# Optimization experiments

Measured on AMD Instinct MI355X. Metric: run time of the kernel, lower is better.

## Reference

```python
import math
import jax, jax.numpy as jnp
import numpy as np

B, C, M = 32, 1024, 1024
D, DV, R_ANCHOR = 512, 512, 64


def setup_inputs() -> dict:
    key = jax.random.key(0)
    ks = jax.random.split(key, 6)
    return {
        "T": jax.random.normal(ks[0], (B, C, M), dtype=jnp.float32),
        "Wq": jax.random.normal(ks[1], (C, D), dtype=jnp.float32) * 0.02,
        "Wk": jax.random.normal(ks[2], (C, D), dtype=jnp.float32) * 0.02,
        "Wv": jax.random.normal(ks[3], (C, DV), dtype=jnp.float32) * 0.02,
        "Wout": jax.random.normal(ks[4], (DV, C), dtype=jnp.float32) * 0.02,
        "R_full": jax.random.normal(ks[5], (R_ANCHOR, M), dtype=jnp.float32) * 0.02,
    }


def reference(T, Wq, Wk, Wv, Wout, R_full):
    # T: [B, C, m] -> tokens-major [B, m, C]
    b, c, m = T.shape
    T_mC = jnp.swapaxes(T, 1, 2)
    Q = T_mC @ Wq           # [B, m, D]
    K = T_mC @ Wk           # [B, m, D]
    V = T_mC @ Wv           # [B, m, DV]
    Rm = R_full[:, :m]      # [r, m]
    # Faithful to original torch einsum: m and j are summed INDEPENDENTLY
    # (outer product of row-sums of R with token-sums of K/V), not contracted.
    K_proj = jnp.einsum('rm,bjd->brd', Rm, K)   # [B, r, D]
    V_proj = jnp.einsum('rm,bjd->brd', Rm, V)   # [B, r, DV]
    scale = 1.0 / math.sqrt(max(1.0, float(Wq.shape[1])))
    scores = jnp.einsum('bid,btd->bit', Q, K_proj) * scale  # [B, m, r]
    A = jax.nn.softmax(scores, axis=-1)
    T_out_mdv = jnp.einsum('bir,brd->bid', A, V_proj)       # [B, m, DV]
    T_out_C = T_out_mdv @ Wout                               # [B, m, C]
    return jnp.swapaxes(T_out_C, 1, 2)                       # [B, C, m]
```

## Files before the change

### kernel.cpp

```cpp
#include <hip/hip_runtime.h>
#include <math.h>

constexpr int Bc  = 32;
constexpr int Cc  = 1024;
constexpr int Mc  = 1024;
constexpr int Dc  = 512;
constexpr int DVc = 512;
constexpr int Rc  = 64;

typedef float f4 __attribute__((ext_vector_type(4)));

__global__ __launch_bounds__(256) void k_kv1(const float* __restrict__ T,
                                             const float* __restrict__ Wk,
                                             const float* __restrict__ Wv,
                                             float* __restrict__ pK,
                                             float* __restrict__ pV) {
    __shared__ float  ts[32];
    __shared__ float4 kp[2][128];
    __shared__ float4 vp[2][128];

    const int cs  = blockIdx.x;
    const int b   = blockIdx.y;
    const int c0  = cs * 32;
    const int tid = threadIdx.x;
    const int w   = tid >> 6, lane = tid & 63;

    const float* Tb = T + ((long)b * Cc + c0 + w * 8) * Mc + lane * 4;
    float racc[8];
#pragma unroll
    for (int rp = 0; rp < 4; ++rp) {
        const float* r0 = Tb + (long)(2 * rp) * Mc;
        const float* r1 = r0 + Mc;
        float4 a[4], c[4];
#pragma unroll
        for (int k = 0; k < 4; ++k) a[k] = *(const float4*)&r0[k * 256];
#pragma unroll
        for (int k = 0; k < 4; ++k) c[k] = *(const float4*)&r1[k * 256];
        float s0 = 0.f, s1 = 0.f;
#pragma unroll
        for (int k = 0; k < 4; ++k) {
            s0 += (a[k].x + a[k].y) + (a[k].z + a[k].w);
            s1 += (c[k].x + c[k].y) + (c[k].z + c[k].w);
        }
        racc[2 * rp] = s0;
        racc[2 * rp + 1] = s1;
    }
#pragma unroll
    for (int off = 32; off; off >>= 1) {
#pragma unroll
        for (int r = 0; r < 8; ++r) racc[r] += __shfl_down(racc[r], off, 64);
    }
    if (lane == 0) {
#pragma unroll
        for (int r = 0; r < 8; ++r) ts[w * 8 + r] = racc[r];
    }
    __syncthreads();

    const int tq = tid >> 7, tr = tid & 127;
    const float4* Wk4 = (const float4*)(Wk + (long)c0 * Dc) + tr;
    const float4* Wv4 = (const float4*)(Wv + (long)c0 * DVc) + tr;
    float4 ka = {0.f, 0.f, 0.f, 0.f}, va = {0.f, 0.f, 0.f, 0.f};
#pragma unroll 4
    for (int j = 0; j < 16; ++j) {
        const int c = j * 2 + tq;
        const float t = ts[c];
        float4 wk = Wk4[(long)c * 128];
        float4 wv = Wv4[(long)c * 128];
        ka.x = fmaf(t, wk.x, ka.x); ka.y = fmaf(t, wk.y, ka.y);
        ka.z = fmaf(t, wk.z, ka.z); ka.w = fmaf(t, wk.w, ka.w);
        va.x = fmaf(t, wv.x, va.x); va.y = fmaf(t, wv.y, va.y);
        va.z = fmaf(t, wv.z, va.z); va.w = fmaf(t, wv.w, va.w);
    }
    kp[tq][tr] = ka;
    vp[tq][tr] = va;
    __syncthreads();

    const long base = ((long)b * 32 + cs) * 512;
    if (tid < 128) {
        float4 s0 = kp[0][tid], s1 = kp[1][tid];
        float4 s = {s0.x + s1.x, s0.y + s1.y, s0.z + s1.z, s0.w + s1.w};
        ((float4*)(pK + base))[tid] = s;
    } else {
        const int t2 = tid - 128;
        float4 s0 = vp[0][t2], s1 = vp[1][t2];
        float4 s = {s0.x + s1.x, s0.y + s1.y, s0.z + s1.z, s0.w + s1.w};
        ((float4*)(pV + base))[t2] = s;
    }
}

__global__ __launch_bounds__(256) void k_kv2r(const float* __restrict__ pK,
                                              const float* __restrict__ pV,
                                              float* __restrict__ Ksum,
                                              float* __restrict__ Vsum,
                                              const float* __restrict__ Rfull,
                                              float* __restrict__ rsum) {
    if (blockIdx.x < 128) {
        const int gid = blockIdx.x * 256 + threadIdx.x;
        const int sel = gid >> 14;
        const int rem = gid & 16383;
        const float* p = (sel ? pV : pK) + (long)(rem >> 9) * 32 * 512 + (rem & 511);
        float v[32];
#pragma unroll
        for (int i = 0; i < 32; ++i) v[i] = p[i * 512];
        float s = 0.f;
#pragma unroll
        for (int i = 0; i < 32; ++i) s += v[i];
        (sel ? Vsum : Ksum)[rem] = s;
    } else {
        const int row  = (blockIdx.x - 128) * 4 + (threadIdx.x >> 6);
        const int lane = threadIdx.x & 63;
        const float* xr = Rfull + (long)row * 1024;
        float s = 0.f;
#pragma unroll
        for (int k = 0; k < 4; ++k) {
            float4 t = *(const float4*)&xr[k * 256 + lane * 4];
            s += (t.x + t.y) + (t.z + t.w);
        }
#pragma unroll
        for (int off = 32; off; off >>= 1) s += __shfl_down(s, off, 64);
        if (lane == 0) rsum[row] = s;
    }
}

__global__ __launch_bounds__(256) void k_mid(const float* __restrict__ Wq,
                                             const float* __restrict__ Ksum,
                                             float* __restrict__ wqk,
                                             const float* __restrict__ Wout,
                                             const float* __restrict__ Vsum,
                                             float* __restrict__ pVW) {
    __shared__ float vs[64];
    if (blockIdx.x < 8192) {
        const int wid  = blockIdx.x * 4 + (threadIdx.x >> 6);
        const int lane = threadIdx.x & 63;
        const float* wq = Wq + (long)(wid & 1023) * Dc;
        const float* ks = Ksum + (wid >> 10) * Dc;
        float s = 0.f;
#pragma unroll
        for (int k = 0; k < 4; ++k) {
            int d = k * 128 + lane * 2;
            float2 a = *(const float2*)&wq[d];
            float2 x = *(const float2*)&ks[d];
            s = fmaf(a.x, x.x, s);
            s = fmaf(a.y, x.y, s);
        }
#pragma unroll
        for (int off = 32; off; off >>= 1) s += __shfl_down(s, off, 64);
        if (lane == 0) wqk[wid] = s;
    } else {
        const int idx = blockIdx.x - 8192;
        const int ds  = idx & 7;
        const int b   = idx >> 3;
        const int d0  = ds * 64;
        const int tid = threadIdx.x;
        if (tid < 64) vs[tid] = Vsum[b * Dc + d0 + tid];
        __syncthreads();
        float a0 = 0.f, a1 = 0.f, a2 = 0.f, a3 = 0.f;
        const float* W0 = Wout + (long)d0 * Cc + tid;
#pragma unroll 4
        for (int d = 0; d < 64; ++d) {
            float v = vs[d];
            const float* wr = W0 + (long)d * Cc;
            a0 = fmaf(v, wr[0],   a0);
            a1 = fmaf(v, wr[256], a1);
            a2 = fmaf(v, wr[512], a2);
            a3 = fmaf(v, wr[768], a3);
        }
        const long base = ((long)b * 8 + ds) * 1024 + tid;
        pVW[base] = a0;  pVW[base + 256] = a1;
        pVW[base + 512] = a2;  pVW[base + 768] = a3;
    }
}

__global__ __launch_bounds__(256) void k_final(const float* __restrict__ T,
                                               const float* __restrict__ wqk,
                                               const float* __restrict__ pVW,
                                               const float* __restrict__ rsum,
                                               float* __restrict__ Out,
                                               float scale) {
    __shared__ float rs[64];
    __shared__ float part[32][40];
    __shared__ float wsh[32];
    __shared__ float wql[Cc];
    __shared__ float vwl[Cc];

    const int b   = blockIdx.y;
    const int m0  = blockIdx.x * 32;
    const int tid = threadIdx.x;
    const int il  = tid & 7;
    const int cs  = tid >> 3;

    ((float4*)wql)[tid] = ((const float4*)(wqk + b * Cc))[tid];
#pragma unroll
    for (int c = tid; c < Cc; c += 256) {
        const float* p = pVW + (long)b * 8 * 1024 + c;
        float v[8];
#pragma unroll
        for (int j = 0; j < 8; ++j) v[j] = p[j * 1024];
        float s = 0.f;
#pragma unroll
        for (int j = 0; j < 8; ++j) s += v[j];
        vwl[c] = s;
    }
    if (tid < 64) rs[tid] = rsum[tid];
    __syncthreads();

    const float* Tbm = T + (long)b * Cc * Mc + m0 + il * 4;
    float4 acc = make_float4(0.f, 0.f, 0.f, 0.f);
#pragma unroll
    for (int cb = 0; cb < 4; ++cb) {
        float4 t[8];
#pragma unroll
        for (int u = 0; u < 8; ++u)
            t[u] = *(const float4*)&Tbm[(long)(cs + (cb * 8 + u) * 32) * Mc];
#pragma unroll
        for (int u = 0; u < 8; ++u) {
            const float wc = wql[cs + (cb * 8 + u) * 32];
            acc.x = fmaf(t[u].x, wc, acc.x);
            acc.y = fmaf(t[u].y, wc, acc.y);
            acc.z = fmaf(t[u].z, wc, acc.z);
            acc.w = fmaf(t[u].w, wc, acc.w);
        }
    }
    *(float4*)&part[cs][il * 4] = acc;
    __syncthreads();

    if (tid < 32) {
        const int i = tid;
        float q = 0.f;
#pragma unroll
        for (int k = 0; k < 32; ++k) q += part[k][i];
        q *= scale;
        float mx = -1e30f;
#pragma unroll
        for (int r = 0; r < 64; ++r) mx = fmaxf(mx, q * rs[r]);
        float se = 0.f, sw = 0.f;
#pragma unroll
        for (int r = 0; r < 64; ++r) {
            float e = __expf(q * rs[r] - mx);
            se += e;
            sw = fmaf(e, rs[r], sw);
        }
        wsh[i] = sw / se;
    }
    __syncthreads();

    float* Ob = Out + (long)b * Cc * Mc + m0 + il * 4;
    float4 w4 = *(const float4*)&wsh[il * 4];
#pragma unroll 4
    for (int c = cs; c < Cc; c += 32) {
        float v = vwl[c];
        f4 o = {w4.x * v, w4.y * v, w4.z * v, w4.w * v};
        __builtin_nontemporal_store(o, (f4*)&Ob[(long)c * Mc]);
    }
}

extern "C" void kernel_launch(void* const* d_in, const int* in_sizes, int n_in,
                              void* d_out, int out_size, void* d_ws, size_t ws_size,
                              hipStream_t stream) {
    const float* T     = (const float*)d_in[0];
    const float* Wq    = (const float*)d_in[1];
    const float* Wk    = (const float*)d_in[2];
    const float* Wv    = (const float*)d_in[3];
    const float* Wout  = (const float*)d_in[4];
    const float* Rfull = (const float*)d_in[5];
    float* Out = (float*)d_out;

    float* ws   = (float*)d_ws;
    float* rsum = ws;
    float* Ksum = rsum + Rc;
    float* Vsum = Ksum + Bc * Dc;
    float* wqk  = Vsum + Bc * DVc;
    float* vw   = wqk + Bc * Cc;
    float* pK   = vw + Bc * Cc;
    float* pV   = pK + 524288;
    float* pVW  = pV + 524288;

    k_kv1<<<dim3(32, Bc), 256, 0, stream>>>(T, Wk, Wv, pK, pV);
    k_kv2r<<<144, 256, 0, stream>>>(pK, pV, Ksum, Vsum, Rfull, rsum);
    k_mid<<<8448, 256, 0, stream>>>(Wq, Ksum, wqk, Wout, Vsum, pVW);
    const float scale = 1.0f / sqrtf((float)Dc);
    k_final<<<dim3(Mc / 32, Bc), 256, 0, stream>>>(T, wqk, pVW, rsum, Out, scale);
}
```

Measured before the change: 285.8 us.

## Fuse KV reduction and mid-stage matvecs into one kernel, drop nontemporal stores

Merges the partial K/V sum reduction, the R row-sum, the Wq·Ksum matvec and the Vsum·Wout matvec into a single kernel with a (9, B) grid. Each block recomputes the per-batch K/V sums in shared memory, so no Ksum/Vsum or pVW partial buffers make a global round trip, and one launch is removed. k_final now loads a finished vw vector instead of summing 8 partials. The final output store also switches from nontemporal to ordinary stores. In exchange, the fused kernel redundantly reduces pK/pV eight times per batch and runs only 288 blocks, which may underuse the GPU.

```diff
diff --git a/kernel.cpp b/kernel.cpp
--- a/kernel.cpp
+++ b/kernel.cpp
@@ -7,8 +7,6 @@
 constexpr int Dc  = 512;
 constexpr int DVc = 512;
 constexpr int Rc  = 64;
-
-typedef float f4 __attribute__((ext_vector_type(4)));
 
 __global__ __launch_bounds__(256) void k_kv1(const float* __restrict__ T,
                                              const float* __restrict__ Wk,
@@ -88,92 +86,122 @@
     }
 }
 
-__global__ __launch_bounds__(256) void k_kv2r(const float* __restrict__ pK,
+__global__ __launch_bounds__(256) void k_mid2(const float* __restrict__ pK,
                                               const float* __restrict__ pV,
-                                              float* __restrict__ Ksum,
-                                              float* __restrict__ Vsum,
+                                              const float* __restrict__ Wq,
+                                              const float* __restrict__ Wout,
                                               const float* __restrict__ Rfull,
+                                              float* __restrict__ wqk,
+                                              float* __restrict__ vw,
                                               float* __restrict__ rsum) {
-    if (blockIdx.x < 128) {
-        const int gid = blockIdx.x * 256 + threadIdx.x;
-        const int sel = gid >> 14;
-        const int rem = gid & 16383;
-        const float* p = (sel ? pV : pK) + (long)(rem >> 9) * 32 * 512 + (rem & 511);
+    __shared__ float Ks[512];
+    __shared__ float Vs[512];
+    __shared__ float pvw[256];
+
+    const int j   = blockIdx.x;
+    const int b   = blockIdx.y;
+    const int tid = threadIdx.x;
+    const int w   = tid >> 6, lane = tid & 63;
+
+    if (j == 8) {
+        if (w < 2) {
+            const int row = 2 * b + w;
+            const float* xr = Rfull + (long)row * 1024;
+            float s = 0.f;
+#pragma unroll
+            for (int k = 0; k < 4; ++k) {
+                float4 t = *(const float4*)&xr[k * 256 + lane * 4];
+                s += (t.x + t.y) + (t.z + t.w);
+            }
+#pragma unroll
+            for (int off = 32; off; off >>= 1) s += __shfl_down(s, off, 64);
+            if (lane == 0) rsum[row] = s;
+        }
+        return;
+    }
+
+    {
+        const float* pKb = pK + (long)b * 32 * 512;
+        const float* pVb = pV + (long)b * 32 * 512;
         float v[32];
 #pragma unroll
-        for (int i = 0; i < 32; ++i) v[i] = p[i * 512];
+        for (int i = 0; i < 32; ++i) v[i] = pKb[i * 512 + tid];
         float s = 0.f;
 #pragma unroll
         for (int i = 0; i < 32; ++i) s += v[i];
-        (sel ? Vsum : Ksum)[rem] = s;
-    } else {
-        const int row  = (blockIdx.x - 128) * 4 + (threadIdx.x >> 6);
-        const int lane = threadIdx.x & 63;
-        const float* xr = Rfull + (long)row * 1024;
-        float s = 0.f;
-#pragma unroll
-        for (int k = 0; k < 4; ++k) {
-            float4 t = *(const float4*)&xr[k * 256 + lane * 4];
-            s += (t.x + t.y) + (t.z + t.w);
-        }
-#pragma unroll
-        for (int off = 32; off; off >>= 1) s += __shfl_down(s, off, 64);
-        if (lane == 0) rsum[row] = s;
-    }
-}
-
-__global__ __launch_bounds__(256) void k_mid(const float* __restrict__ Wq,
-                                             const float* __restrict__ Ksum,
-                                             float* __restrict__ wqk,
-                                             const float* __restrict__ Wout,
-                                             const float* __restrict__ Vsum,
-                                             float* __restrict__ pVW) {
-    __shared__ float vs[64];
-    if (blockIdx.x < 8192) {
-        const int wid  = blockIdx.x * 4 + (threadIdx.x >> 6);
-        const int lane = threadIdx.x & 63;
-        const float* wq = Wq + (long)(wid & 1023) * Dc;
-        const float* ks = Ksum + (wid >> 10) * Dc;
-        float s = 0.f;
-#pragma unroll
-        for (int k = 0; k < 4; ++k) {
-            int d = k * 128 + lane * 2;
-            float2 a = *(const float2*)&wq[d];
-            float2 x = *(const float2*)&ks[d];
-            s = fmaf(a.x, x.x, s);
-            s = fmaf(a.y, x.y, s);
-        }
-#pragma unroll
-        for (int off = 32; off; off >>= 1) s += __shfl_down(s, off, 64);
-        if (lane == 0) wqk[wid] = s;
-    } else {
-        const int idx = blockIdx.x - 8192;
-        const int ds  = idx & 7;
-        const int b   = idx >> 3;
-        const int d0  = ds * 64;
-        const int tid = threadIdx.x;
-        if (tid < 64) vs[tid] = Vsum[b * Dc + d0 + tid];
+        Ks[tid] = s;
+#pragma unroll
+        for (int i = 0; i < 32; ++i) v[i] = pKb[i * 512 + tid + 256];
+        s = 0.f;
+#pragma unroll
+        for (int i = 0; i < 32; ++i) s += v[i];
+        Ks[tid + 256] = s;
+#pragma unroll
+        for (int i = 0; i < 32; ++i) v[i] = pVb[i * 512 + tid];
+        s = 0.f;
+#pragma unroll
+        for (int i = 0; i < 32; ++i) s += v[i];
+        Vs[tid] = s;
+#pragma unroll
+        for (int i = 0; i < 32; ++i) v[i] = pVb[i * 512 + tid + 256];
+        s = 0.f;
+#pragma unroll
+        for (int i = 0; i < 32; ++i) s += v[i];
+        Vs[tid + 256] = s;
+    }
+    __syncthreads();
+
+    const int c0 = j * 128;
+
+    {
+        float myKs[8];
+#pragma unroll
+        for (int k = 0; k < 8; ++k) myKs[k] = Ks[lane + k * 64];
+        const int cbase = c0 + w * 32;
+#pragma unroll
+        for (int bt = 0; bt < 4; ++bt) {
+            float p[8];
+#pragma unroll
+            for (int u = 0; u < 8; ++u) {
+                const float* wqr = Wq + (long)(cbase + bt * 8 + u) * Dc + lane;
+                float acc = 0.f;
+#pragma unroll
+                for (int k = 0; k < 8; ++k) acc = fmaf(wqr[k * 64], myKs[k], acc);
+                p[u] = acc;
+            }
+#pragma unroll
+            for (int off = 32; off; off >>= 1) {
+#pragma unroll
+                for (int u = 0; u < 8; ++u) p[u] += __shfl_down(p[u], off, 64);
+            }
+            if (lane == 0) {
+#pragma unroll
+                for (int u = 0; u < 8; ++u) wqk[b * Cc + cbase + bt * 8 + u] = p[u];
+            }
+        }
+    }
+
+    {
+        const int ci = tid & 127, h = tid >> 7;
+        const float* W0 = Wout + (long)(h * 256) * Cc + c0 + ci;
+        float acc = 0.f;
+#pragma unroll 4
+        for (int d0 = 0; d0 < 256; d0 += 8) {
+            float w8[8];
+#pragma unroll
+            for (int q = 0; q < 8; ++q) w8[q] = W0[(long)(d0 + q) * Cc];
+#pragma unroll
+            for (int q = 0; q < 8; ++q) acc = fmaf(Vs[h * 256 + d0 + q], w8[q], acc);
+        }
+        pvw[tid] = acc;
         __syncthreads();
-        float a0 = 0.f, a1 = 0.f, a2 = 0.f, a3 = 0.f;
-        const float* W0 = Wout + (long)d0 * Cc + tid;
-#pragma unroll 4
-        for (int d = 0; d < 64; ++d) {
-            float v = vs[d];
-            const float* wr = W0 + (long)d * Cc;
-            a0 = fmaf(v, wr[0],   a0);
-            a1 = fmaf(v, wr[256], a1);
-            a2 = fmaf(v, wr[512], a2);
-            a3 = fmaf(v, wr[768], a3);
-        }
-        const long base = ((long)b * 8 + ds) * 1024 + tid;
-        pVW[base] = a0;  pVW[base + 256] = a1;
-        pVW[base + 512] = a2;  pVW[base + 768] = a3;
+        if (tid < 128) vw[b * Cc + c0 + tid] = pvw[tid] + pvw[tid + 128];
     }
 }
 
 __global__ __launch_bounds__(256) void k_final(const float* __restrict__ T,
                                                const float* __restrict__ wqk,
-                                               const float* __restrict__ pVW,
+                                               const float* __restrict__ vw,
                                                const float* __restrict__ rsum,
                                                float* __restrict__ Out,
                                                float scale) {
@@ -190,17 +218,7 @@
     const int cs  = tid >> 3;
 
     ((float4*)wql)[tid] = ((const float4*)(wqk + b * Cc))[tid];
-#pragma unroll
-    for (int c = tid; c < Cc; c += 256) {
-        const float* p = pVW + (long)b * 8 * 1024 + c;
-        float v[8];
-#pragma unroll
-        for (int j = 0; j < 8; ++j) v[j] = p[j * 1024];
-        float s = 0.f;
-#pragma unroll
-        for (int j = 0; j < 8; ++j) s += v[j];
-        vwl[c] = s;
-    }
+    ((float4*)vwl)[tid] = ((const float4*)(vw  + b * Cc))[tid];
     if (tid < 64) rs[tid] = rsum[tid];
     __syncthreads();
 
@@ -249,8 +267,8 @@
 #pragma unroll 4
     for (int c = cs; c < Cc; c += 32) {
         float v = vwl[c];
-        f4 o = {w4.x * v, w4.y * v, w4.z * v, w4.w * v};
-        __builtin_nontemporal_store(o, (f4*)&Ob[(long)c * Mc]);
+        *(float4*)&Ob[(long)c * Mc] =
+            make_float4(w4.x * v, w4.y * v, w4.z * v, w4.w * v);
     }
 }
 
@@ -267,17 +285,13 @@
 
     float* ws   = (float*)d_ws;
     float* rsum = ws;
-    float* Ksum = rsum + Rc;
-    float* Vsum = Ksum + Bc * Dc;
-    float* wqk  = Vsum + Bc * DVc;
+    float* wqk  = rsum + Rc + 32768;
     float* vw   = wqk + Bc * Cc;
     float* pK   = vw + Bc * Cc;
     float* pV   = pK + 524288;
-    float* pVW  = pV + 524288;
 
     k_kv1<<<dim3(32, Bc), 256, 0, stream>>>(T, Wk, Wv, pK, pV);
-    k_kv2r<<<144, 256, 0, stream>>>(pK, pV, Ksum, Vsum, Rfull, rsum);
-    k_mid<<<8448, 256, 0, stream>>>(Wq, Ksum, wqk, Wout, Vsum, pVW);
+    k_mid2<<<dim3(9, Bc), 256, 0, stream>>>(pK, pV, Wq, Wout, Rfull, wqk, vw, rsum);
     const float scale = 1.0f / sqrtf((float)Dc);
-    k_final<<<dim3(Mc / 32, Bc), 256, 0, stream>>>(T, wqk, pVW, rsum, Out, scale);
-}
+    k_final<<<dim3(32, Bc), 256, 0, stream>>>(T, wqk, vw, rsum, Out, scale);
+}
```

Result: slower. 307.1 us (+7.5%).
